# Kernel optimization log

Measured on AMD Instinct MI355X. Metric: run time of the kernel, lower is better.

## Reference

```python
import jax, jax.numpy as jnp
import numpy as np

D_M = 1024
NUM_TOK = 4096


def setup_inputs() -> dict:
    key = jax.random.key(0)
    ks = jax.random.split(key, 7)
    mk = lambda k, shp: jax.random.normal(k, shp, dtype=jnp.float32) * 0.02
    return {
        "X": jax.random.normal(ks[0], (D_M, NUM_TOK), dtype=jnp.float32),
        "W_Q": mk(ks[1], (D_M, D_M)),
        "W_K": mk(ks[2], (D_M, D_M)),
        "W_V": mk(ks[3], (D_M, D_M)),
        "W_O": mk(ks[4], (D_M, D_M)),
        "mlp_in": mk(ks[5], (D_M, D_M)),
        "mlp_out": mk(ks[6], (D_M, D_M)),
    }


def reference(X, W_Q, W_K, W_V, W_O, mlp_in, mlp_out):
    # X: [d_m, num_tok]; module transposes to tokens-major [N, d]
    Xt = X.T  # [N, d]
    N = Xt.shape[0]
    Q = Xt @ W_Q  # [N, d]
    K = Xt @ W_K  # [N, d]
    scores = Q @ K.T  # [N, N] -- NOTE: no 1/sqrt(d) scaling, as in the original
    causal = jnp.tril(jnp.ones((N, N), dtype=bool))  # keep lower triangle incl. diag
    scores = jnp.where(causal, scores, -jnp.inf)
    A = jax.nn.softmax(scores, axis=-1)  # [N, N]
    # original applies W_V then W_O to X BEFORE the attention mix
    RH = (Xt @ W_V) @ W_O  # [N, d]
    Xt = Xt + A @ RH  # residual + attention
    h = jax.nn.relu(Xt @ mlp_in)  # [N, d] (hidden dim == d_m in original)
    Xt = Xt + h @ mlp_out  # residual + MLP
    return Xt.T  # back to [d_m, num_tok]
```

## Files before the change

kernel.cpp:

```cpp
#include <hip/hip_runtime.h>
#include <stdint.h>
#include <stddef.h>

using f16 = _Float16;
typedef __attribute__((ext_vector_type(8))) _Float16 f16x8;
typedef __attribute__((ext_vector_type(4))) float f32x4;

__device__ __forceinline__ void async_copy16(const f16* g, f16* l) {
    __builtin_amdgcn_global_load_lds(
        (const __attribute__((address_space(1))) void*)g,
        (__attribute__((address_space(3))) void*)l, 16, 0, 0);
}

template <int N>
__device__ __forceinline__ void wait_vmcnt() {
    if constexpr (N == 0)       asm volatile("s_waitcnt vmcnt(0)" ::: "memory");
    else if constexpr (N == 6)  asm volatile("s_waitcnt vmcnt(6)" ::: "memory");
    else if constexpr (N == 8)  asm volatile("s_waitcnt vmcnt(8)" ::: "memory");
    else if constexpr (N == 12) asm volatile("s_waitcnt vmcnt(12)" ::: "memory");
}

__device__ __forceinline__ void hard_barrier() {
    __builtin_amdgcn_sched_barrier(0);
    __builtin_amdgcn_s_barrier();
    __builtin_amdgcn_sched_barrier(0);
}

__global__ __launch_bounds__(256)
void prep_w(const float* __restrict__ w0, const float* __restrict__ w1,
            const float* __restrict__ w2, const float* __restrict__ w3,
            const float* __restrict__ w4, const float* __restrict__ w5,
            f16* o0, f16* o1, f16* o2, f16* o3, f16* o4, f16* o5, int D) {
    __shared__ float tile[32][33];
    const int tx = threadIdx.x & 31, ty = threadIdx.x >> 5;
    const int b = blockIdx.x;
    const int z = b >> 10, r = b & 1023;
    const float* in = z == 0 ? w0 : z == 1 ? w1 : z == 2 ? w2 : z == 3 ? w3 : z == 4 ? w4 : w5;
    f16* out = z == 0 ? o0 : z == 1 ? o1 : z == 2 ? o2 : z == 3 ? o3 : z == 4 ? o4 : o5;
    const int c0 = (r & 31) * 32, r0 = (r >> 5) * 32;
    if (z < 3) {
#pragma unroll
        for (int j = 0; j < 4; j++) {
            size_t idx = (size_t)(r0 + ty + j * 8) * D + c0 + tx;
            out[idx] = (f16)in[idx];
        }
    } else {
#pragma unroll
        for (int j = 0; j < 4; j++)
            tile[ty + j * 8][tx] = in[(size_t)(r0 + ty + j * 8) * D + c0 + tx];
        __syncthreads();
#pragma unroll
        for (int j = 0; j < 4; j++)
            out[(size_t)(c0 + ty + j * 8) * D + r0 + tx] = (f16)tile[tx][ty + j * 8];
    }
}

__device__ __forceinline__ void body64db(
    f16* lds, const f16* __restrict__ A, const f16* __restrict__ B,
    f16* __restrict__ Ch, int m0, int n0, int N, int K, int lda) {
    const int t = threadIdx.x;
    const int lane = t & 63, wave = t >> 6;
    const int wm = (wave >> 1) * 32, wn = (wave & 1) * 32;
    const int lm = lane & 15, lq = lane >> 4;
    const int srow = t >> 2;
    const int gs = ((t & 3) ^ ((srow >> 1) & 3)) * 8;
    const int rs = (lq ^ ((lm >> 1) & 3)) * 8;

    auto stage = [&](f16* buf, int k0) {
#pragma unroll
        for (int r = 0; r < 4; r++)
            async_copy16(A + (size_t)(m0 + srow) * lda + k0 + r * 32 + gs,
                         buf + r * 2048 + t * 8);
#pragma unroll
        for (int r = 0; r < 4; r++)
            async_copy16(B + (size_t)(n0 + srow) * K + k0 + r * 32 + gs,
                         buf + 8192 + r * 2048 + t * 8);
    };

    f32x4 acc[2][2] = {};
    stage(lds, 0);
    __syncthreads();
    int cur = 0;
    for (int k0 = 0; k0 < K; k0 += 128) {
        f16* cb = lds + cur * 16384;
        if (k0 + 128 < K) stage(lds + (cur ^ 1) * 16384, k0 + 128);
#pragma unroll
        for (int kk = 0; kk < 4; kk++) {
            f16x8 af[2], bf[2];
#pragma unroll
            for (int i = 0; i < 2; i++)
                af[i] = *(const f16x8*)&cb[kk * 2048 + (wm + i * 16 + lm) * 32 + rs];
#pragma unroll
            for (int j = 0; j < 2; j++)
                bf[j] = *(const f16x8*)&cb[8192 + kk * 2048 + (wn + j * 16 + lm) * 32 + rs];
#pragma unroll
            for (int i = 0; i < 2; i++)
#pragma unroll
                for (int j = 0; j < 2; j++)
                    acc[i][j] = __builtin_amdgcn_mfma_f32_16x16x32_f16(
                        af[i], bf[j], acc[i][j], 0, 0, 0);
        }
        __syncthreads();
        cur ^= 1;
    }

#pragma unroll
    for (int i = 0; i < 2; i++) {
        const int row = m0 + wm + i * 16 + lq * 4;
#pragma unroll
        for (int j = 0; j < 2; j++) {
            const int col = n0 + wn + j * 16 + lm;
            f32x4 v = acc[i][j];
#pragma unroll
            for (int r = 0; r < 4; r++)
                Ch[(size_t)(row + r) * N + col] = (f16)v[r];
        }
    }
}

__global__ __launch_bounds__(256, 2)
void prepx_tiny(const float* __restrict__ X, f16* __restrict__ Xth,
                const f16* Wkh, const f16* Wqh, f16* GT,
                const f16* Wot, const f16* Wvh, f16* HT, int D, int NT) {
    __shared__ alignas(16) f16 smem[32768];
    int b = blockIdx.x;
    if (b < 4096) {
        float* tile = (float*)smem;
        const int tx = threadIdx.x & 31, ty = threadIdx.x >> 5;
        const int c0 = (b & 127) * 32, r0 = (b >> 7) * 32;
#pragma unroll
        for (int j = 0; j < 4; j++)
            tile[(ty + j * 8) * 33 + tx] = X[(size_t)(r0 + ty + j * 8) * NT + c0 + tx];
        __syncthreads();
#pragma unroll
        for (int j = 0; j < 4; j++)
            Xth[(size_t)(c0 + ty + j * 8) * D + r0 + tx] = (f16)tile[tx * 33 + ty + j * 8];
        return;
    }
    b -= 4096;
    if (b < 256)
        body64db(smem, Wkh, Wqh, GT, (b >> 4) * 64, (b & 15) * 64, 1024, 1024, 1024);
    else {
        const int r = b - 256;
        body64db(smem, Wot, Wvh, HT, (r >> 4) * 64, (r & 15) * 64, 1024, 1024, 1024);
    }
}

__global__ __launch_bounds__(256)
void softmax_rows(f16* __restrict__ A, int N) {
    const int row = blockIdx.x, len = row + 1;
    const int lim = ((row >> 7) + 1) << 7;
    f16* a = A + (size_t)row * N;
    __shared__ float red[256];
    const int t = threadIdx.x;

    float v[16];
    float mx = -1e30f;
#pragma unroll
    for (int j = 0; j < 2; j++) {
        const int c = (t + j * 256) * 8;
        if (c < len) {
            f16x8 x = *(const f16x8*)(a + c);
#pragma unroll
            for (int e = 0; e < 8; e++) {
                float f = (c + e < len) ? (float)x[e] : -1e30f;
                v[j * 8 + e] = f;
                mx = fmaxf(mx, f);
            }
        } else {
#pragma unroll
            for (int e = 0; e < 8; e++) v[j * 8 + e] = -1e30f;
        }
    }
    red[t] = mx; __syncthreads();
    for (int o = 128; o > 0; o >>= 1) { if (t < o) red[t] = fmaxf(red[t], red[t + o]); __syncthreads(); }
    mx = red[0]; __syncthreads();

    float sum = 0.f;
#pragma unroll
    for (int k = 0; k < 16; k++) {
        float e = (v[k] > -1e29f) ? __expf(v[k] - mx) : 0.0f;
        v[k] = e;
        sum += e;
    }
    red[t] = sum; __syncthreads();
    for (int o = 128; o > 0; o >>= 1) { if (t < o) red[t] += red[t + o]; __syncthreads(); }
    const float inv = 1.0f / red[0];
#pragma unroll
    for (int j = 0; j < 2; j++) {
        const int c = (t + j * 256) * 8;
        if (c < lim) {
            f16x8 o8;
#pragma unroll
            for (int e = 0; e < 8; e++) o8[e] = (f16)(v[j * 8 + e] * inv);
            *(f16x8*)(a + c) = o8;
        }
    }
}


__device__ __forceinline__ void body128sq(
    f16* lds, const f16* __restrict__ A, const f16* __restrict__ B,
    f16* __restrict__ Ch, int m0, int n0, int N, int K, int lda) {
    constexpr int BUF = 16384;
    const int t = threadIdx.x;
    const int lane = t & 63, wave = t >> 6;
    const int wm = (wave >> 1) * 64, wn = (wave & 1) * 64;
    const int lm = lane & 15, lq = lane >> 4;
    const int srow = t >> 2;
    const int gs = ((t & 3) ^ ((srow >> 1) & 3)) * 8;
    const int rs = (lq ^ ((lm >> 1) & 3)) * 8;

    f32x4 acc[4][4] = {};

    auto stage = [&](f16* buf, int k0) {
#pragma unroll
        for (int r = 0; r < 4; r++)
            async_copy16(A + (size_t)(m0 + (r & 1) * 64 + srow) * lda + k0 + (r >> 1) * 32 + gs,
                         buf + r * 2048 + t * 8);
#pragma unroll
        for (int r = 0; r < 4; r++)
            async_copy16(B + (size_t)(n0 + (r & 1) * 64 + srow) * K + k0 + (r >> 1) * 32 + gs,
                         buf + 8192 + r * 2048 + t * 8);
    };

    auto compute = [&](const f16* cb) {
#pragma unroll
        for (int kk = 0; kk < 2; kk++) {
            f16x8 af[4], bf[4];
#pragma unroll
            for (int i = 0; i < 4; i++)
                af[i] = *(const f16x8*)&cb[kk * 4096 + (wm + i * 16 + lm) * 32 + rs];
#pragma unroll
            for (int j = 0; j < 4; j++)
                bf[j] = *(const f16x8*)&cb[8192 + kk * 4096 + (wn + j * 16 + lm) * 32 + rs];
#pragma unroll
            for (int i = 0; i < 4; i++)
#pragma unroll
                for (int j = 0; j < 4; j++)
                    acc[i][j] = __builtin_amdgcn_mfma_f32_16x16x32_f16(
                        af[i], bf[j], acc[i][j], 0, 0, 0);
        }
    };

    const int NS = K >> 6;
    stage(lds, 0);
    for (int s = 0; s < NS; s++) {
        if (s + 1 < NS) {
            stage(lds + ((s + 1) & 1) * BUF, (s + 1) << 6);
            wait_vmcnt<8>();
        } else {
            wait_vmcnt<0>();
        }
        hard_barrier();
        compute(lds + (s & 1) * BUF);
        if (s + 1 < NS) hard_barrier();
    }

#pragma unroll
    for (int i = 0; i < 4; i++) {
        const int row = m0 + wm + i * 16 + lq * 4;
#pragma unroll
        for (int j = 0; j < 4; j++) {
            const int col = n0 + wn + j * 16 + lm;
            f32x4 v = acc[i][j];
#pragma unroll
            for (int r = 0; r < 4; r++)
                Ch[(size_t)(row + r) * N + col] = (f16)v[r];
        }
    }
}

template <int MODE>
__device__ __forceinline__ void body_pf2(
    f16* lds, const f16* __restrict__ A, const f16* __restrict__ B,
    float* __restrict__ Cf, f16* __restrict__ Ch, const f16* __restrict__ resid,
    int m0, int n0, int M, int N, int K, int lda, int Keff) {
    constexpr int ASZ = 128 * 64;
    constexpr int BSZ = 64 * 64;
    constexpr int SSZ = ASZ + BSZ;
    const int t = threadIdx.x;
    const int lane = t & 63, wave = t >> 6;
    const int wm = (wave >> 1) * 64, wn = (wave & 1) * 32;
    const int lm = lane & 15, lq = lane >> 4;
    const int srow = t >> 2;
    const int gs = ((t & 3) ^ ((srow >> 1) & 3)) * 8;
    const int rs = (lq ^ ((lm >> 1) & 3)) * 8;

    f32x4 acc[4][2] = {};

    auto stage = [&](f16* buf, int k0) {
#pragma unroll
        for (int r = 0; r < 4; r++)
            async_copy16(A + (size_t)(m0 + (r & 1) * 64 + srow) * lda + k0 + (r >> 1) * 32 + gs,
                         buf + r * 2048 + t * 8);
#pragma unroll
        for (int r = 0; r < 2; r++)
            async_copy16(B + (size_t)(n0 + srow) * K + k0 + r * 32 + gs,
                         buf + ASZ + r * 2048 + t * 8);
    };

    auto compute = [&](const f16* cb) {
#pragma unroll
        for (int kk = 0; kk < 2; kk++) {
            f16x8 af[4], bf[2];
#pragma unroll
            for (int i = 0; i < 4; i++)
                af[i] = *(const f16x8*)&cb[kk * 4096 + (wm + i * 16 + lm) * 32 + rs];
#pragma unroll
            for (int j = 0; j < 2; j++)
                bf[j] = *(const f16x8*)&cb[ASZ + kk * 2048 + (wn + j * 16 + lm) * 32 + rs];
#pragma unroll
            for (int i = 0; i < 4; i++)
#pragma unroll
                for (int j = 0; j < 2; j++)
                    acc[i][j] = __builtin_amdgcn_mfma_f32_16x16x32_f16(
                        af[i], bf[j], acc[i][j], 0, 0, 0);
        }
    };

    f16 *pa = lds, *pb = lds + SSZ, *pc = lds + 2 * SSZ;
    stage(pa, 0);
    stage(pb, 64);
    const int NS = Keff >> 6;
    for (int s = 0; s < NS; s++) {
        const int k2 = (s + 2) << 6;
        if (k2 < Keff) {
            stage(pc, k2);
            wait_vmcnt<12>();
        } else if (s + 1 < NS) {
            wait_vmcnt<6>();
        } else {
            wait_vmcnt<0>();
        }
        hard_barrier();
        compute(pa);
        hard_barrier();
        f16* tp = pa; pa = pb; pb = pc; pc = tp;
    }

#pragma unroll
    for (int i = 0; i < 4; i++) {
        const int row = m0 + wm + i * 16 + lq * 4;
#pragma unroll
        for (int j = 0; j < 2; j++) {
            const int col = n0 + wn + j * 16 + lm;
            f32x4 v = acc[i][j];
#pragma unroll
            for (int r = 0; r < 4; r++) {
                if (MODE == 0) {
                    Ch[(size_t)(row + r) * N + col] = (f16)v[r];
                } else if (MODE == 2) {
                    float o = v[r] + (float)resid[(size_t)(row + r) * N + col];
                    Ch[(size_t)(row + r) * N + col] = (f16)o;
                } else if (MODE == 3) {
                    Ch[(size_t)(row + r) * N + col] = (f16)fmaxf(v[r], 0.0f);
                } else {
                    float o = v[r] + (float)resid[(size_t)(row + r) * N + col];
                    Cf[(size_t)col * M + (row + r)] = o;
                }
            }
        }
    }
}

__global__ __launch_bounds__(256, 2)
void midq(const f16* Xth, const f16* GT, f16* Qp) {
    __shared__ alignas(16) f16 smem[36864];
    const int x = blockIdx.x & 7, s = blockIdx.x >> 3;
    const int m = x + 8 * (s >> 4), n = s & 15;
    body_pf2<0>(smem, Xth, GT, nullptr, Qp, nullptr,
                m * 128, n * 64, 4096, 1024, 1024, 1024, 1024);
}

__global__ __launch_bounds__(256, 2)
void scores_midrh(const f16* Qp, const f16* Xth, f16* Af,
                  const f16* HT, f16* RHt) {
    __shared__ alignas(16) f16 smem[32768];
    int b = blockIdx.x;
    if (b < 528) {
        const int x = b & 7;
        int s = b >> 3;
        int m = 0, n = 0;
#pragma unroll
        for (int q = 3; q >= 0; q--) {
            const int mm = 8 * q + ((q & 1) ? 7 - x : x);
            if (s < mm + 1) { m = mm; n = s; break; }
            s -= mm + 1;
        }
        body128sq(smem, Qp, Xth, Af, m * 128, n * 128, 4096, 1024, 1024);
    } else {
        const int r = b - 528;
        const int x = r & 7;
        const int s = r >> 3;
        const int n = x + 8 * (s >> 3), m = s & 7;
        body128sq(smem, HT, Xth, RHt, m * 128, n * 128, 4096, 1024, 1024);
    }
}

template <int MODE, bool CAUSAL_K>
__global__ __launch_bounds__(256, 2)
void gemm_nar(const f16* __restrict__ A, const f16* __restrict__ B,
              float* __restrict__ Cf, f16* __restrict__ Ch,
              const f16* __restrict__ resid, int M, int N, int K, int lda) {
    __shared__ alignas(16) f16 smem[36864];
    const int x = blockIdx.x & 7, s = blockIdx.x >> 3;
    const int qs = s >> 4, n = s & 15;
    int m;
    if (CAUSAL_K) {
        const int q = (qs == 0) ? 3 : (qs == 1) ? 2 : (qs == 2) ? 0 : 1;
        m = 8 * q + ((q & 1) ? 7 - x : x);
    } else {
        m = x + 8 * qs;
    }
    const int m0 = m * 128, n0 = n * 64;
    int Keff = K;
    if (CAUSAL_K) {
        Keff = m0 + 128;
        if (Keff > K) Keff = K;
    }
    body_pf2<MODE>(smem, A, B, Cf, Ch, resid,
                   m0, n0, M, N, K, lda, Keff);
}

extern "C" void kernel_launch(void* const* d_in, const int* in_sizes, int n_in,
                              void* d_out, int out_size, void* d_ws, size_t ws_size,
                              hipStream_t stream) {
    const int D = 1024, NT = 4096;
    const float* X = (const float*)d_in[0];
    const float* W[6] = {(const float*)d_in[1], (const float*)d_in[2],
                         (const float*)d_in[3], (const float*)d_in[4],
                         (const float*)d_in[5], (const float*)d_in[6]};
    char* ws = (char*)d_ws;
    auto MB = [](size_t x) { return x << 20; };

    f16*   Xth  = (f16*)(ws + MB(0));
    f16*   Wqh  = (f16*)(ws + MB(8));
    f16*   Wkh  = (f16*)(ws + MB(10));
    f16*   Wvh  = (f16*)(ws + MB(12));
    f16*   Wot  = (f16*)(ws + MB(14));
    f16*   W4t  = (f16*)(ws + MB(16));
    f16*   W5t  = (f16*)(ws + MB(18));
    f16*   GT   = (f16*)(ws + MB(20));
    f16*   HT   = (f16*)(ws + MB(22));
    f16*   Qp   = (f16*)(ws + MB(24));
    f16*   Af   = (f16*)(ws + MB(32));
    f16*   RHt  = (f16*)(ws + MB(64));
    f16*   Y1h  = (f16*)(ws + MB(72));
    f16*   hb   = (f16*)(ws + MB(24));
    float* outF = (float*)d_out;

    prep_w<<<6144, 256, 0, stream>>>(W[0], W[1], W[2], W[3], W[4], W[5],
                                     Wqh, Wkh, Wvh, Wot, W4t, W5t, D);

    prepx_tiny<<<4608, 256, 0, stream>>>(X, Xth, Wkh, Wqh, GT, Wot, Wvh, HT,
                                         D, NT);

    midq<<<512, 256, 0, stream>>>(Xth, GT, Qp);

    scores_midrh<<<784, 256, 0, stream>>>(Qp, Xth, Af, HT, RHt);

    softmax_rows<<<NT, 256, 0, stream>>>(Af, NT);

    gemm_nar<2, true><<<512, 256, 0, stream>>>(
        Af, RHt, nullptr, Y1h, Xth, NT, D, NT, NT);

    gemm_nar<3, false><<<512, 256, 0, stream>>>(
        Y1h, W4t, nullptr, hb, nullptr, NT, D, D, D);

    gemm_nar<4, false><<<512, 256, 0, stream>>>(
        hb, W5t, outF, nullptr, Y1h, NT, D, D, D);
}
```

Baseline: 230.2 us.

## Drop multi-stage LDS prefetch in GEMM bodies, single-buffer for higher occupancy

Replaces the double-buffered (body128sq) and triple-buffered (body_pf2) async global-to-LDS prefetch pipelines with a simple single-buffer loop. Each step loads one K-slice, synchronizes, computes, then synchronizes again. Shared memory per block shrinks, and launch bounds rise from 2 to 3 blocks per CU, trading software prefetch overlap for more resident waves. The risk is that global load latency is no longer hidden within a block and now relies only on other blocks being resident.

```diff
diff --git a/kernel.cpp b/kernel.cpp
--- a/kernel.cpp
+++ b/kernel.cpp
@@ -10,20 +10,6 @@
     __builtin_amdgcn_global_load_lds(
         (const __attribute__((address_space(1))) void*)g,
         (__attribute__((address_space(3))) void*)l, 16, 0, 0);
-}
-
-template <int N>
-__device__ __forceinline__ void wait_vmcnt() {
-    if constexpr (N == 0)       asm volatile("s_waitcnt vmcnt(0)" ::: "memory");
-    else if constexpr (N == 6)  asm volatile("s_waitcnt vmcnt(6)" ::: "memory");
-    else if constexpr (N == 8)  asm volatile("s_waitcnt vmcnt(8)" ::: "memory");
-    else if constexpr (N == 12) asm volatile("s_waitcnt vmcnt(12)" ::: "memory");
-}
-
-__device__ __forceinline__ void hard_barrier() {
-    __builtin_amdgcn_sched_barrier(0);
-    __builtin_amdgcn_s_barrier();
-    __builtin_amdgcn_sched_barrier(0);
 }
 
 __global__ __launch_bounds__(256)
@@ -202,7 +188,6 @@
 __device__ __forceinline__ void body128sq(
     f16* lds, const f16* __restrict__ A, const f16* __restrict__ B,
     f16* __restrict__ Ch, int m0, int n0, int N, int K, int lda) {
-    constexpr int BUF = 16384;
     const int t = threadIdx.x;
     const int lane = t & 63, wave = t >> 6;
     const int wm = (wave >> 1) * 64, wn = (wave & 1) * 64;
@@ -213,27 +198,27 @@
 
     f32x4 acc[4][4] = {};
 
-    auto stage = [&](f16* buf, int k0) {
+    const int NS = K >> 6;
+    for (int s = 0; s < NS; s++) {
+        const int k0 = s << 6;
 #pragma unroll
         for (int r = 0; r < 4; r++)
             async_copy16(A + (size_t)(m0 + (r & 1) * 64 + srow) * lda + k0 + (r >> 1) * 32 + gs,
-                         buf + r * 2048 + t * 8);
+                         lds + r * 2048 + t * 8);
 #pragma unroll
         for (int r = 0; r < 4; r++)
             async_copy16(B + (size_t)(n0 + (r & 1) * 64 + srow) * K + k0 + (r >> 1) * 32 + gs,
-                         buf + 8192 + r * 2048 + t * 8);
-    };
-
-    auto compute = [&](const f16* cb) {
+                         lds + 8192 + r * 2048 + t * 8);
+        __syncthreads();
 #pragma unroll
         for (int kk = 0; kk < 2; kk++) {
             f16x8 af[4], bf[4];
 #pragma unroll
             for (int i = 0; i < 4; i++)
-                af[i] = *(const f16x8*)&cb[kk * 4096 + (wm + i * 16 + lm) * 32 + rs];
+                af[i] = *(const f16x8*)&lds[kk * 4096 + (wm + i * 16 + lm) * 32 + rs];
 #pragma unroll
             for (int j = 0; j < 4; j++)
-                bf[j] = *(const f16x8*)&cb[8192 + kk * 4096 + (wn + j * 16 + lm) * 32 + rs];
+                bf[j] = *(const f16x8*)&lds[8192 + kk * 4096 + (wn + j * 16 + lm) * 32 + rs];
 #pragma unroll
             for (int i = 0; i < 4; i++)
 #pragma unroll
@@ -241,20 +226,7 @@
                     acc[i][j] = __builtin_amdgcn_mfma_f32_16x16x32_f16(
                         af[i], bf[j], acc[i][j], 0, 0, 0);
         }
-    };
-
-    const int NS = K >> 6;
-    stage(lds, 0);
-    for (int s = 0; s < NS; s++) {
-        if (s + 1 < NS) {
-            stage(lds + ((s + 1) & 1) * BUF, (s + 1) << 6);
-            wait_vmcnt<8>();
-        } else {
-            wait_vmcnt<0>();
-        }
-        hard_barrier();
-        compute(lds + (s & 1) * BUF);
-        if (s + 1 < NS) hard_barrier();
+        if (s + 1 < NS) __syncthreads();
     }
 
 #pragma unroll
@@ -272,13 +244,11 @@
 }
 
 template <int MODE>
-__device__ __forceinline__ void body_pf2(
+__device__ __forceinline__ void body_nar(
     f16* lds, const f16* __restrict__ A, const f16* __restrict__ B,
     float* __restrict__ Cf, f16* __restrict__ Ch, const f16* __restrict__ resid,
     int m0, int n0, int M, int N, int K, int lda, int Keff) {
     constexpr int ASZ = 128 * 64;
-    constexpr int BSZ = 64 * 64;
-    constexpr int SSZ = ASZ + BSZ;
     const int t = threadIdx.x;
     const int lane = t & 63, wave = t >> 6;
     const int wm = (wave >> 1) * 64, wn = (wave & 1) * 32;
@@ -289,27 +259,27 @@
 
     f32x4 acc[4][2] = {};
 
-    auto stage = [&](f16* buf, int k0) {
+    const int NS = Keff >> 6;
+    for (int s = 0; s < NS; s++) {
+        const int k0 = s << 6;
 #pragma unroll
         for (int r = 0; r < 4; r++)
             async_copy16(A + (size_t)(m0 + (r & 1) * 64 + srow) * lda + k0 + (r >> 1) * 32 + gs,
-                         buf + r * 2048 + t * 8);
+                         lds + r * 2048 + t * 8);
 #pragma unroll
         for (int r = 0; r < 2; r++)
             async_copy16(B + (size_t)(n0 + srow) * K + k0 + r * 32 + gs,
-                         buf + ASZ + r * 2048 + t * 8);
-    };
-
-    auto compute = [&](const f16* cb) {
+                         lds + ASZ + r * 2048 + t * 8);
+        __syncthreads();
 #pragma unroll
         for (int kk = 0; kk < 2; kk++) {
             f16x8 af[4], bf[2];
 #pragma unroll
             for (int i = 0; i < 4; i++)
-                af[i] = *(const f16x8*)&cb[kk * 4096 + (wm + i * 16 + lm) * 32 + rs];
+                af[i] = *(const f16x8*)&lds[kk * 4096 + (wm + i * 16 + lm) * 32 + rs];
 #pragma unroll
             for (int j = 0; j < 2; j++)
-                bf[j] = *(const f16x8*)&cb[ASZ + kk * 2048 + (wn + j * 16 + lm) * 32 + rs];
+                bf[j] = *(const f16x8*)&lds[ASZ + kk * 2048 + (wn + j * 16 + lm) * 32 + rs];
 #pragma unroll
             for (int i = 0; i < 4; i++)
 #pragma unroll
@@ -317,26 +287,7 @@
                     acc[i][j] = __builtin_amdgcn_mfma_f32_16x16x32_f16(
                         af[i], bf[j], acc[i][j], 0, 0, 0);
         }
-    };
-
-    f16 *pa = lds, *pb = lds + SSZ, *pc = lds + 2 * SSZ;
-    stage(pa, 0);
-    stage(pb, 64);
-    const int NS = Keff >> 6;
-    for (int s = 0; s < NS; s++) {
-        const int k2 = (s + 2) << 6;
-        if (k2 < Keff) {
-            stage(pc, k2);
-            wait_vmcnt<12>();
-        } else if (s + 1 < NS) {
-            wait_vmcnt<6>();
-        } else {
-            wait_vmcnt<0>();
-        }
-        hard_barrier();
-        compute(pa);
-        hard_barrier();
-        f16* tp = pa; pa = pb; pb = pc; pc = tp;
+        if (s + 1 < NS) __syncthreads();
     }
 
 #pragma unroll
@@ -364,19 +315,19 @@
     }
 }
 
-__global__ __launch_bounds__(256, 2)
+__global__ __launch_bounds__(256, 3)
 void midq(const f16* Xth, const f16* GT, f16* Qp) {
-    __shared__ alignas(16) f16 smem[36864];
+    __shared__ alignas(16) f16 smem[12288];
     const int x = blockIdx.x & 7, s = blockIdx.x >> 3;
     const int m = x + 8 * (s >> 4), n = s & 15;
-    body_pf2<0>(smem, Xth, GT, nullptr, Qp, nullptr,
+    body_nar<0>(smem, Xth, GT, nullptr, Qp, nullptr,
                 m * 128, n * 64, 4096, 1024, 1024, 1024, 1024);
 }
 
-__global__ __launch_bounds__(256, 2)
+__global__ __launch_bounds__(256, 3)
 void scores_midrh(const f16* Qp, const f16* Xth, f16* Af,
                   const f16* HT, f16* RHt) {
-    __shared__ alignas(16) f16 smem[32768];
+    __shared__ alignas(16) f16 smem[16384];
     int b = blockIdx.x;
     if (b < 528) {
         const int x = b & 7;
@@ -399,11 +350,11 @@
 }
 
 template <int MODE, bool CAUSAL_K>
-__global__ __launch_bounds__(256, 2)
+__global__ __launch_bounds__(256, 3)
 void gemm_nar(const f16* __restrict__ A, const f16* __restrict__ B,
               float* __restrict__ Cf, f16* __restrict__ Ch,
               const f16* __restrict__ resid, int M, int N, int K, int lda) {
-    __shared__ alignas(16) f16 smem[36864];
+    __shared__ alignas(16) f16 smem[12288];
     const int x = blockIdx.x & 7, s = blockIdx.x >> 3;
     const int qs = s >> 4, n = s & 15;
     int m;
@@ -419,7 +370,7 @@
         Keff = m0 + 128;
         if (Keff > K) Keff = K;
     }
-    body_pf2<MODE>(smem, A, B, Cf, Ch, resid,
+    body_nar<MODE>(smem, A, B, Cf, Ch, resid,
                    m0, n0, M, N, K, lda, Keff);
 }
 
```

Result: slower. 259.3 us (+12.6%).

## Rebalance kernel work: move RH GEMM into softmax launch and MLP weight prep into prepx

Applied to the files above, without the earlier changes.

Moves the RHt GEMM blocks out of the scores kernel into the softmax kernel, so they run alongside the memory-bound softmax rows. Those blocks use a new single-buffered 128x128 GEMM body that fits the softmax kernel's smaller LDS allocation. The transposes of the two MLP weights move from prep_w into prepx_tiny, so they overlap with the X transpose and the small weight-product GEMMs. The aim is better load balance and fewer tail gaps between kernels, at the cost of a less pipelined RH GEMM and mixed block types within one launch.

```diff
diff --git a/kernel.cpp b/kernel.cpp
--- a/kernel.cpp
+++ b/kernel.cpp
@@ -29,14 +29,13 @@
 __global__ __launch_bounds__(256)
 void prep_w(const float* __restrict__ w0, const float* __restrict__ w1,
             const float* __restrict__ w2, const float* __restrict__ w3,
-            const float* __restrict__ w4, const float* __restrict__ w5,
-            f16* o0, f16* o1, f16* o2, f16* o3, f16* o4, f16* o5, int D) {
+            f16* o0, f16* o1, f16* o2, f16* o3, int D) {
     __shared__ float tile[32][33];
     const int tx = threadIdx.x & 31, ty = threadIdx.x >> 5;
     const int b = blockIdx.x;
     const int z = b >> 10, r = b & 1023;
-    const float* in = z == 0 ? w0 : z == 1 ? w1 : z == 2 ? w2 : z == 3 ? w3 : z == 4 ? w4 : w5;
-    f16* out = z == 0 ? o0 : z == 1 ? o1 : z == 2 ? o2 : z == 3 ? o3 : z == 4 ? o4 : o5;
+    const float* in = z == 0 ? w0 : z == 1 ? w1 : z == 2 ? w2 : w3;
+    f16* out = z == 0 ? o0 : z == 1 ? o1 : z == 2 ? o2 : o3;
     const int c0 = (r & 31) * 32, r0 = (r >> 5) * 32;
     if (z < 3) {
 #pragma unroll
@@ -120,13 +119,15 @@
 
 __global__ __launch_bounds__(256, 2)
 void prepx_tiny(const float* __restrict__ X, f16* __restrict__ Xth,
+                const float* __restrict__ w4, const float* __restrict__ w5,
+                f16* W4t, f16* W5t,
                 const f16* Wkh, const f16* Wqh, f16* GT,
                 const f16* Wot, const f16* Wvh, f16* HT, int D, int NT) {
     __shared__ alignas(16) f16 smem[32768];
     int b = blockIdx.x;
+    const int tx = threadIdx.x & 31, ty = threadIdx.x >> 5;
     if (b < 4096) {
         float* tile = (float*)smem;
-        const int tx = threadIdx.x & 31, ty = threadIdx.x >> 5;
         const int c0 = (b & 127) * 32, r0 = (b >> 7) * 32;
 #pragma unroll
         for (int j = 0; j < 4; j++)
@@ -138,6 +139,22 @@
         return;
     }
     b -= 4096;
+    if (b < 2048) {
+        float* tile = (float*)smem;
+        const float* in = (b < 1024) ? w4 : w5;
+        f16* out = (b < 1024) ? W4t : W5t;
+        const int r = b & 1023;
+        const int c0 = (r & 31) * 32, r0 = (r >> 5) * 32;
+#pragma unroll
+        for (int j = 0; j < 4; j++)
+            tile[(ty + j * 8) * 33 + tx] = in[(size_t)(r0 + ty + j * 8) * D + c0 + tx];
+        __syncthreads();
+#pragma unroll
+        for (int j = 0; j < 4; j++)
+            out[(size_t)(c0 + ty + j * 8) * D + r0 + tx] = (f16)tile[tx * 33 + ty + j * 8];
+        return;
+    }
+    b -= 2048;
     if (b < 256)
         body64db(smem, Wkh, Wqh, GT, (b >> 4) * 64, (b & 15) * 64, 1024, 1024, 1024);
     else {
@@ -146,60 +163,8 @@
     }
 }
 
-__global__ __launch_bounds__(256)
-void softmax_rows(f16* __restrict__ A, int N) {
-    const int row = blockIdx.x, len = row + 1;
-    const int lim = ((row >> 7) + 1) << 7;
-    f16* a = A + (size_t)row * N;
-    __shared__ float red[256];
-    const int t = threadIdx.x;
-
-    float v[16];
-    float mx = -1e30f;
-#pragma unroll
-    for (int j = 0; j < 2; j++) {
-        const int c = (t + j * 256) * 8;
-        if (c < len) {
-            f16x8 x = *(const f16x8*)(a + c);
-#pragma unroll
-            for (int e = 0; e < 8; e++) {
-                float f = (c + e < len) ? (float)x[e] : -1e30f;
-                v[j * 8 + e] = f;
-                mx = fmaxf(mx, f);
-            }
-        } else {
-#pragma unroll
-            for (int e = 0; e < 8; e++) v[j * 8 + e] = -1e30f;
-        }
-    }
-    red[t] = mx; __syncthreads();
-    for (int o = 128; o > 0; o >>= 1) { if (t < o) red[t] = fmaxf(red[t], red[t + o]); __syncthreads(); }
-    mx = red[0]; __syncthreads();
-
-    float sum = 0.f;
-#pragma unroll
-    for (int k = 0; k < 16; k++) {
-        float e = (v[k] > -1e29f) ? __expf(v[k] - mx) : 0.0f;
-        v[k] = e;
-        sum += e;
-    }
-    red[t] = sum; __syncthreads();
-    for (int o = 128; o > 0; o >>= 1) { if (t < o) red[t] += red[t + o]; __syncthreads(); }
-    const float inv = 1.0f / red[0];
-#pragma unroll
-    for (int j = 0; j < 2; j++) {
-        const int c = (t + j * 256) * 8;
-        if (c < lim) {
-            f16x8 o8;
-#pragma unroll
-            for (int e = 0; e < 8; e++) o8[e] = (f16)(v[j * 8 + e] * inv);
-            *(f16x8*)(a + c) = o8;
-        }
-    }
-}
-
-
-__device__ __forceinline__ void body128sq(
+
+__device__ __forceinline__ void body128sq_db(
     f16* lds, const f16* __restrict__ A, const f16* __restrict__ B,
     f16* __restrict__ Ch, int m0, int n0, int N, int K, int lda) {
     constexpr int BUF = 16384;
@@ -255,6 +220,64 @@
         hard_barrier();
         compute(lds + (s & 1) * BUF);
         if (s + 1 < NS) hard_barrier();
+    }
+
+#pragma unroll
+    for (int i = 0; i < 4; i++) {
+        const int row = m0 + wm + i * 16 + lq * 4;
+#pragma unroll
+        for (int j = 0; j < 4; j++) {
+            const int col = n0 + wn + j * 16 + lm;
+            f32x4 v = acc[i][j];
+#pragma unroll
+            for (int r = 0; r < 4; r++)
+                Ch[(size_t)(row + r) * N + col] = (f16)v[r];
+        }
+    }
+}
+
+__device__ __forceinline__ void body128sq_1b(
+    f16* lds, const f16* __restrict__ A, const f16* __restrict__ B,
+    f16* __restrict__ Ch, int m0, int n0, int N, int K, int lda) {
+    const int t = threadIdx.x;
+    const int lane = t & 63, wave = t >> 6;
+    const int wm = (wave >> 1) * 64, wn = (wave & 1) * 64;
+    const int lm = lane & 15, lq = lane >> 4;
+    const int srow = t >> 2;
+    const int gs = ((t & 3) ^ ((srow >> 1) & 3)) * 8;
+    const int rs = (lq ^ ((lm >> 1) & 3)) * 8;
+
+    f32x4 acc[4][4] = {};
+
+    const int NS = K >> 6;
+    for (int s = 0; s < NS; s++) {
+        const int k0 = s << 6;
+#pragma unroll
+        for (int r = 0; r < 4; r++)
+            async_copy16(A + (size_t)(m0 + (r & 1) * 64 + srow) * lda + k0 + (r >> 1) * 32 + gs,
+                         lds + r * 2048 + t * 8);
+#pragma unroll
+        for (int r = 0; r < 4; r++)
+            async_copy16(B + (size_t)(n0 + (r & 1) * 64 + srow) * K + k0 + (r >> 1) * 32 + gs,
+                         lds + 8192 + r * 2048 + t * 8);
+        __syncthreads();
+#pragma unroll
+        for (int kk = 0; kk < 2; kk++) {
+            f16x8 af[4], bf[4];
+#pragma unroll
+            for (int i = 0; i < 4; i++)
+                af[i] = *(const f16x8*)&lds[kk * 4096 + (wm + i * 16 + lm) * 32 + rs];
+#pragma unroll
+            for (int j = 0; j < 4; j++)
+                bf[j] = *(const f16x8*)&lds[8192 + kk * 4096 + (wn + j * 16 + lm) * 32 + rs];
+#pragma unroll
+            for (int i = 0; i < 4; i++)
+#pragma unroll
+                for (int j = 0; j < 4; j++)
+                    acc[i][j] = __builtin_amdgcn_mfma_f32_16x16x32_f16(
+                        af[i], bf[j], acc[i][j], 0, 0, 0);
+        }
+        if (s + 1 < NS) __syncthreads();
     }
 
 #pragma unroll
@@ -374,27 +397,80 @@
 }
 
 __global__ __launch_bounds__(256, 2)
-void scores_midrh(const f16* Qp, const f16* Xth, f16* Af,
-                  const f16* HT, f16* RHt) {
+void scores_tri(const f16* Qp, const f16* Xth, f16* Af) {
     __shared__ alignas(16) f16 smem[32768];
+    const int x = blockIdx.x & 7;
+    int s = blockIdx.x >> 3;
+    int m = 0, n = 0;
+#pragma unroll
+    for (int q = 3; q >= 0; q--) {
+        const int mm = 8 * q + ((q & 1) ? 7 - x : x);
+        if (s < mm + 1) { m = mm; n = s; break; }
+        s -= mm + 1;
+    }
+    body128sq_db(smem, Qp, Xth, Af, m * 128, n * 128, 4096, 1024, 1024);
+}
+
+__global__ __launch_bounds__(256)
+void softmax_midrh(f16* __restrict__ A, int N,
+                   const f16* HT, const f16* Xth, f16* RHt) {
+    __shared__ alignas(16) f16 smem[16384];
     int b = blockIdx.x;
-    if (b < 528) {
-        const int x = b & 7;
-        int s = b >> 3;
-        int m = 0, n = 0;
-#pragma unroll
-        for (int q = 3; q >= 0; q--) {
-            const int mm = 8 * q + ((q & 1) ? 7 - x : x);
-            if (s < mm + 1) { m = mm; n = s; break; }
-            s -= mm + 1;
-        }
-        body128sq(smem, Qp, Xth, Af, m * 128, n * 128, 4096, 1024, 1024);
-    } else {
-        const int r = b - 528;
+    if (b >= 4096) {
+        const int r = b - 4096;
         const int x = r & 7;
         const int s = r >> 3;
         const int n = x + 8 * (s >> 3), m = s & 7;
-        body128sq(smem, HT, Xth, RHt, m * 128, n * 128, 4096, 1024, 1024);
+        body128sq_1b(smem, HT, Xth, RHt, m * 128, n * 128, 4096, 1024, 1024);
+        return;
+    }
+    const int row = b, len = row + 1;
+    const int lim = ((row >> 7) + 1) << 7;
+    f16* a = A + (size_t)row * N;
+    float* red = (float*)smem;
+    const int t = threadIdx.x;
+
+    float v[16];
+    float mx = -1e30f;
+#pragma unroll
+    for (int j = 0; j < 2; j++) {
+        const int c = (t + j * 256) * 8;
+        if (c < len) {
+            f16x8 x = *(const f16x8*)(a + c);
+#pragma unroll
+            for (int e = 0; e < 8; e++) {
+                float f = (c + e < len) ? (float)x[e] : -1e30f;
+                v[j * 8 + e] = f;
+                mx = fmaxf(mx, f);
+            }
+        } else {
+#pragma unroll
+            for (int e = 0; e < 8; e++) v[j * 8 + e] = -1e30f;
+        }
+    }
+    red[t] = mx; __syncthreads();
+    for (int o = 128; o > 0; o >>= 1) { if (t < o) red[t] = fmaxf(red[t], red[t + o]); __syncthreads(); }
+    mx = red[0]; __syncthreads();
+
+    float sum = 0.f;
+#pragma unroll
+    for (int k = 0; k < 16; k++) {
+        float e = (v[k] > -1e29f) ? __expf(v[k] - mx) : 0.0f;
+        v[k] = e;
+        sum += e;
+    }
+    red[t] = sum; __syncthreads();
+    for (int o = 128; o > 0; o >>= 1) { if (t < o) red[t] += red[t + o]; __syncthreads(); }
+    const float inv = 1.0f / red[0];
+#pragma unroll
+    for (int j = 0; j < 2; j++) {
+        const int c = (t + j * 256) * 8;
+        if (c < lim) {
+            f16x8 o8;
+#pragma unroll
+            for (int e = 0; e < 8; e++) o8[e] = (f16)(v[j * 8 + e] * inv);
+            *(f16x8*)(a + c) = o8;
+        }
     }
 }
 
@@ -450,17 +526,17 @@
     f16*   hb   = (f16*)(ws + MB(24));
     float* outF = (float*)d_out;
 
-    prep_w<<<6144, 256, 0, stream>>>(W[0], W[1], W[2], W[3], W[4], W[5],
-                                     Wqh, Wkh, Wvh, Wot, W4t, W5t, D);
-
-    prepx_tiny<<<4608, 256, 0, stream>>>(X, Xth, Wkh, Wqh, GT, Wot, Wvh, HT,
-                                         D, NT);
+    prep_w<<<4096, 256, 0, stream>>>(W[0], W[1], W[2], W[3],
+                                     Wqh, Wkh, Wvh, Wot, D);
+
+    prepx_tiny<<<6656, 256, 0, stream>>>(X, Xth, W[4], W[5], W4t, W5t,
+                                         Wkh, Wqh, GT, Wot, Wvh, HT, D, NT);
 
     midq<<<512, 256, 0, stream>>>(Xth, GT, Qp);
 
-    scores_midrh<<<784, 256, 0, stream>>>(Qp, Xth, Af, HT, RHt);
-
-    softmax_rows<<<NT, 256, 0, stream>>>(Af, NT);
+    scores_tri<<<528, 256, 0, stream>>>(Qp, Xth, Af);
+
+    softmax_midrh<<<4352, 256, 0, stream>>>(Af, NT, HT, Xth, RHt);
 
     gemm_nar<2, true><<<512, 256, 0, stream>>>(
         Af, RHt, nullptr, Y1h, Xth, NT, D, NT, NT);
```

New measurement: 244.6 us. +6.2%, slower.
